# Kernel optimization log

Measured on AMD Instinct MI355X. Metric: run time of the kernel, lower is better.

## Reference

```python
import jax, jax.numpy as jnp
import numpy as np
from jax.scipy.linalg import expm

PROTO_M = 0.99  # hparams['ema_ratio']
NUM_CLASSES = 1000
OUT_DIM = 512
BATCH = 16384


def setup_inputs() -> dict:
    key = jax.random.key(0)
    k1, k2, k3, k4, k5, k6, k7 = jax.random.split(key, 7)
    f = jax.random.normal(k1, (BATCH, OUT_DIM), dtype=jnp.float32)
    f_aug = jax.random.normal(k2, (BATCH, OUT_DIM), dtype=jnp.float32)
    y = jax.random.randint(k3, (BATCH,), 0, NUM_CLASSES, dtype=jnp.int32)
    prototypes = jax.random.normal(k4, (NUM_CLASSES, OUT_DIM), dtype=jnp.float32)
    prototypes_y = jax.random.normal(k5, (NUM_CLASSES, OUT_DIM), dtype=jnp.float32)
    # small positive weights so expm(W*W) stays well-conditioned (DAG weights start near 0)
    weight_pos = jax.random.uniform(k6, (OUT_DIM + 1, OUT_DIM + 1), dtype=jnp.float32) * 0.05
    weight_neg = jax.random.uniform(k7, (OUT_DIM + 1, OUT_DIM + 1), dtype=jnp.float32) * 0.05
    return {"f": f, "f_aug": f_aug, "y": y, "prototypes": prototypes,
            "prototypes_y": prototypes_y, "weight_pos": weight_pos, "weight_neg": weight_neg}


def _l2norm(x, axis=-1, eps=1e-12):
    return x / jnp.maximum(jnp.linalg.norm(x, axis=axis, keepdims=True), eps)


def _ema_scatter(proto, feats, y, num_classes, m):
    # Exact closed form of the sequential per-sample EMA loop:
    # proto_new[c] = proto[c] * m^count(c) + sum_{i: y_i=c} (1-m) * m^{#later same-label} * feats[i]
    B = feats.shape[0]
    onehot = jax.nn.one_hot(y, num_classes, dtype=feats.dtype)          # [B, C]
    counts = onehot.sum(axis=0)                                          # [C]
    cum = jnp.cumsum(onehot, axis=0)                                     # inclusive counts [B, C]
    suffix = counts[y] - cum[jnp.arange(B), y]                           # later same-label count [B]
    w = (1.0 - m) * (m ** suffix)                                        # per-sample EMA weight [B]
    proto_new = proto * (m ** counts)[:, None]
    proto_new = proto_new.at[y].add(w[:, None] * feats)
    return proto_new


def reference(f, f_aug, y, prototypes, prototypes_y, weight_pos, weight_neg):
    D = f.shape[1]
    # dag_mlp mask: expm((W_pos - W_neg)^2)[:dims, -1]
    W = weight_pos - weight_neg
    E = expm(W * W)
    mask = E[:D, -1]                     # [D]
    masked_f_aug = f_aug * mask[None, :]
    nf = _l2norm(f, axis=1)
    nmfa = _l2norm(masked_f_aug, axis=1)
    C = prototypes.shape[0]
    p = _ema_scatter(prototypes, nf, y, C, PROTO_M)
    py = _ema_scatter(prototypes_y, nmfa, y, C, PROTO_M)
    p = _l2norm(p, axis=1)
    py = _l2norm(py, axis=1)
    return (p, py)
```

## Files before the change

kernel.cpp:

```cpp
#include <hip/hip_runtime.h>

#define DP1   513
#define ODIM  512
#define NCLS  1000
#define BATCH 16384
#define MAXC  64
#define MAXW  64
#define L2M   (-0.014499569695115089f)

__global__ __launch_bounds__(256) void mask_kernel(const float* __restrict__ wp,
                                                   const float* __restrict__ wn,
                                                   float* __restrict__ mask) {
    const int wv = threadIdx.x >> 6, lane = threadIdx.x & 63;
    const int i = blockIdx.x * 4 + wv;
    const size_t ro = (size_t)i * DP1;
    float acc = 0.0f;
    for (int j = lane; j < DP1; j += 64) {
        const float w  = wp[ro + j] - wn[ro + j];
        const float wj = wp[(size_t)j * DP1 + (DP1 - 1)] - wn[(size_t)j * DP1 + (DP1 - 1)];
        acc = fmaf(w * w, wj * wj, acc);
    }
#pragma unroll
    for (int off = 32; off > 0; off >>= 1) acc += __shfl_xor(acc, off, 64);
    if (lane == 0) {
        const float w = wp[ro + DP1 - 1] - wn[ro + DP1 - 1];
        mask[i] = fmaf(0.5f, acc, w * w);
    }
}

__global__ __launch_bounds__(256, 4)
void class_kernel(const float* __restrict__ f,
                  const float* __restrict__ f_aug,
                  const int* __restrict__ y,
                  const float* __restrict__ protos,
                  const float* __restrict__ protos_y,
                  const float* __restrict__ mask,
                  float* __restrict__ out) {
    const int c = blockIdx.x;
    const int t = threadIdx.x;
    const int lane = t & 63;
    const int wv = t >> 6;

    __shared__ int   wl[4][MAXW];
    __shared__ int   wcnt[4];
    __shared__ int   s_rows[MAXC];
    __shared__ int   s_off[4], s_cnt;
    __shared__ float sP[4][ODIM], sQ[4][ODIM];
    __shared__ float redA[4], redB[4];

    {
        const unsigned long long mlt = (lane == 0) ? 0ull : ((~0ull) >> (64 - lane));
        int running = 0;
        for (int it = 0; it < 16; ++it) {
            const int base = wv * 4096 + it * 256;
            const int4 yv = ((const int4*)(y + base))[lane];
            const unsigned long long b0 = __ballot(yv.x == c);
            const unsigned long long b1 = __ballot(yv.y == c);
            const unsigned long long b2 = __ballot(yv.z == c);
            const unsigned long long b3 = __ballot(yv.w == c);
            const int cl = __popcll(b0 & mlt) + __popcll(b1 & mlt)
                         + __popcll(b2 & mlt) + __popcll(b3 & mlt);
            int same = 0;
            if (yv.x == c) { int r = running + cl + same; if (r < MAXW) wl[wv][r] = base + 4 * lane + 0; same++; }
            if (yv.y == c) { int r = running + cl + same; if (r < MAXW) wl[wv][r] = base + 4 * lane + 1; same++; }
            if (yv.z == c) { int r = running + cl + same; if (r < MAXW) wl[wv][r] = base + 4 * lane + 2; same++; }
            if (yv.w == c) { int r = running + cl + same; if (r < MAXW) wl[wv][r] = base + 4 * lane + 3; same++; }
            running += __popcll(b0) + __popcll(b1) + __popcll(b2) + __popcll(b3);
        }
        if (lane == 0) wcnt[wv] = (running < MAXW) ? running : MAXW;
    }
    __syncthreads();
    if (t == 0) {
        int o = 0;
#pragma unroll
        for (int w = 0; w < 4; ++w) { s_off[w] = o; o += wcnt[w]; }
        s_cnt = (o < MAXC) ? o : MAXC;
    }
    __syncthreads();
    const int cnt = s_cnt;
    {
        const int o = s_off[wv], n = wcnt[wv];
        for (int k = lane; k < n; k += 64) {
            const int g = o + k;
            if (g < MAXC) s_rows[g] = wl[wv][k];
        }
    }
    __syncthreads();

    const float4 m0 = ((const float4*)mask)[lane];
    const float4 m1 = ((const float4*)mask)[lane + 64];
    float4 aP0 = {0,0,0,0}, aP1 = {0,0,0,0};
    float4 aQ0 = {0,0,0,0}, aQ1 = {0,0,0,0};

    for (int j = wv; j < cnt; j += 4) {
        const int row = s_rows[j];
        const float4* fr = (const float4*)(f + (size_t)row * ODIM);
        const float4* gr = (const float4*)(f_aug + (size_t)row * ODIM);
        const float4 a0 = fr[lane], a1 = fr[lane + 64];
        const float4 g0 = gr[lane], g1 = gr[lane + 64];
        float sA = a0.x*a0.x + a0.y*a0.y + a0.z*a0.z + a0.w*a0.w
                 + a1.x*a1.x + a1.y*a1.y + a1.z*a1.z + a1.w*a1.w;
        const float c0 = g0.x*m0.x, c1 = g0.y*m0.y, c2 = g0.z*m0.z, c3 = g0.w*m0.w;
        const float c4 = g1.x*m1.x, c5 = g1.y*m1.y, c6 = g1.z*m1.z, c7 = g1.w*m1.w;
        float sB = c0*c0 + c1*c1 + c2*c2 + c3*c3 + c4*c4 + c5*c5 + c6*c6 + c7*c7;
#pragma unroll
        for (int off = 32; off > 0; off >>= 1) {
            sA += __shfl_xor(sA, off, 64);
            sB += __shfl_xor(sB, off, 64);
        }
        const float w  = 0.01f * __builtin_exp2f((float)(cnt - 1 - j) * L2M);
        const float wA = w / fmaxf(sqrtf(sA), 1e-12f);
        const float wB = w / fmaxf(sqrtf(sB), 1e-12f);
        aP0.x = fmaf(a0.x, wA, aP0.x); aP0.y = fmaf(a0.y, wA, aP0.y);
        aP0.z = fmaf(a0.z, wA, aP0.z); aP0.w = fmaf(a0.w, wA, aP0.w);
        aP1.x = fmaf(a1.x, wA, aP1.x); aP1.y = fmaf(a1.y, wA, aP1.y);
        aP1.z = fmaf(a1.z, wA, aP1.z); aP1.w = fmaf(a1.w, wA, aP1.w);
        aQ0.x = fmaf(g0.x, wB, aQ0.x); aQ0.y = fmaf(g0.y, wB, aQ0.y);
        aQ0.z = fmaf(g0.z, wB, aQ0.z); aQ0.w = fmaf(g0.w, wB, aQ0.w);
        aQ1.x = fmaf(g1.x, wB, aQ1.x); aQ1.y = fmaf(g1.y, wB, aQ1.y);
        aQ1.z = fmaf(g1.z, wB, aQ1.z); aQ1.w = fmaf(g1.w, wB, aQ1.w);
    }
    ((float4*)sP[wv])[lane]      = aP0;
    ((float4*)sP[wv])[lane + 64] = aP1;
    ((float4*)sQ[wv])[lane]      = aQ0;
    ((float4*)sQ[wv])[lane + 64] = aQ1;
    __syncthreads();

    float P0 = 0.0f, P1 = 0.0f, Q0 = 0.0f, Q1 = 0.0f;
#pragma unroll
    for (int w = 0; w < 4; ++w) {
        P0 += sP[w][t]; P1 += sP[w][t + 256];
        Q0 += sQ[w][t]; Q1 += sQ[w][t + 256];
    }
    const float mc = __builtin_exp2f((float)cnt * L2M);
    const float p0 = fmaf(protos[(size_t)c * ODIM + t],         mc, P0);
    const float p1 = fmaf(protos[(size_t)c * ODIM + t + 256],   mc, P1);
    const float q0 = fmaf(protos_y[(size_t)c * ODIM + t],       mc, mask[t] * Q0);
    const float q1 = fmaf(protos_y[(size_t)c * ODIM + t + 256], mc, mask[t + 256] * Q1);

    float sPn = fmaf(p0, p0, p1 * p1);
    float sQn = fmaf(q0, q0, q1 * q1);
#pragma unroll
    for (int off = 32; off > 0; off >>= 1) {
        sPn += __shfl_xor(sPn, off, 64);
        sQn += __shfl_xor(sQn, off, 64);
    }
    if (lane == 0) { redA[wv] = sPn; redB[wv] = sQn; }
    __syncthreads();
    const float ssP = redA[0] + redA[1] + redA[2] + redA[3];
    const float ssQ = redB[0] + redB[1] + redB[2] + redB[3];
    const float iP = 1.0f / fmaxf(sqrtf(ssP), 1e-12f);
    const float iQ = 1.0f / fmaxf(sqrtf(ssQ), 1e-12f);
    out[(size_t)c * ODIM + t]                       = p0 * iP;
    out[(size_t)c * ODIM + t + 256]                 = p1 * iP;
    out[(size_t)(NCLS + c) * ODIM + t]              = q0 * iQ;
    out[(size_t)(NCLS + c) * ODIM + t + 256]        = q1 * iQ;
}

extern "C" void kernel_launch(void* const* d_in, const int* in_sizes, int n_in,
                              void* d_out, int out_size, void* d_ws, size_t ws_size,
                              hipStream_t stream) {
    const float* f       = (const float*)d_in[0];
    const float* f_aug   = (const float*)d_in[1];
    const int*   y       = (const int*)d_in[2];
    const float* protos  = (const float*)d_in[3];
    const float* protosy = (const float*)d_in[4];
    const float* wp      = (const float*)d_in[5];
    const float* wn      = (const float*)d_in[6];
    float* out = (float*)d_out;

    float* mask = (float*)d_ws;

    mask_kernel<<<128, 256, 0, stream>>>(wp, wn, mask);
    class_kernel<<<NCLS, 256, 0, stream>>>(f, f_aug, y, protos, protosy, mask, out);
}
```

Before: 29.81 us.

## Process each wave's own sample list with prefetch and per-wave EMA scaling

Each wave now accumulates only the samples it found in its own quarter of the batch, so the cross-wave offset computation, the merged row list and two block barriers are removed. EMA weights are built incrementally within a wave by multiplying by 1/m per step and rescaled per wave at the final reduction using the counts of the later waves. The next row's f and f_aug are loaded one iteration ahead to hide global load latency, and the label scan loop is unrolled. The incremental power product can drift slightly from the exact exponent, and the per-wave work is unbalanced when labels cluster in one quarter of the batch.

Result: slower. 32.61 us (+9.4%).

```diff
diff --git a/kernel.cpp b/kernel.cpp
--- a/kernel.cpp
+++ b/kernel.cpp
@@ -4,7 +4,6 @@
 #define ODIM  512
 #define NCLS  1000
 #define BATCH 16384
-#define MAXC  64
 #define MAXW  64
 #define L2M   (-0.014499569695115089f)
 
@@ -43,14 +42,14 @@
 
     __shared__ int   wl[4][MAXW];
     __shared__ int   wcnt[4];
-    __shared__ int   s_rows[MAXC];
-    __shared__ int   s_off[4], s_cnt;
     __shared__ float sP[4][ODIM], sQ[4][ODIM];
     __shared__ float redA[4], redB[4];
 
+    int nw;
     {
         const unsigned long long mlt = (lane == 0) ? 0ull : ((~0ull) >> (64 - lane));
         int running = 0;
+#pragma unroll
         for (int it = 0; it < 16; ++it) {
             const int base = wv * 4096 + it * 256;
             const int4 yv = ((const int4*)(y + base))[lane];
@@ -67,58 +66,53 @@
             if (yv.w == c) { int r = running + cl + same; if (r < MAXW) wl[wv][r] = base + 4 * lane + 3; same++; }
             running += __popcll(b0) + __popcll(b1) + __popcll(b2) + __popcll(b3);
         }
-        if (lane == 0) wcnt[wv] = (running < MAXW) ? running : MAXW;
+        nw = (running < MAXW) ? running : MAXW;
+        if (lane == 0) wcnt[wv] = nw;
     }
-    __syncthreads();
-    if (t == 0) {
-        int o = 0;
-#pragma unroll
-        for (int w = 0; w < 4; ++w) { s_off[w] = o; o += wcnt[w]; }
-        s_cnt = (o < MAXC) ? o : MAXC;
-    }
-    __syncthreads();
-    const int cnt = s_cnt;
-    {
-        const int o = s_off[wv], n = wcnt[wv];
-        for (int k = lane; k < n; k += 64) {
-            const int g = o + k;
-            if (g < MAXC) s_rows[g] = wl[wv][k];
-        }
-    }
-    __syncthreads();
 
     const float4 m0 = ((const float4*)mask)[lane];
     const float4 m1 = ((const float4*)mask)[lane + 64];
     float4 aP0 = {0,0,0,0}, aP1 = {0,0,0,0};
     float4 aQ0 = {0,0,0,0}, aQ1 = {0,0,0,0};
 
-    for (int j = wv; j < cnt; j += 4) {
-        const int row = s_rows[j];
+    if (nw > 0) {
+        int row = wl[wv][0];
         const float4* fr = (const float4*)(f + (size_t)row * ODIM);
         const float4* gr = (const float4*)(f_aug + (size_t)row * ODIM);
-        const float4 a0 = fr[lane], a1 = fr[lane + 64];
-        const float4 g0 = gr[lane], g1 = gr[lane + 64];
-        float sA = a0.x*a0.x + a0.y*a0.y + a0.z*a0.z + a0.w*a0.w
-                 + a1.x*a1.x + a1.y*a1.y + a1.z*a1.z + a1.w*a1.w;
-        const float c0 = g0.x*m0.x, c1 = g0.y*m0.y, c2 = g0.z*m0.z, c3 = g0.w*m0.w;
-        const float c4 = g1.x*m1.x, c5 = g1.y*m1.y, c6 = g1.z*m1.z, c7 = g1.w*m1.w;
-        float sB = c0*c0 + c1*c1 + c2*c2 + c3*c3 + c4*c4 + c5*c5 + c6*c6 + c7*c7;
+        float4 A0 = fr[lane], A1 = fr[lane + 64];
+        float4 G0 = gr[lane], G1 = gr[lane + 64];
+        float pw = 1.0f;
+        const float pinc = 1.0101010101010102f;
+        for (int j = 0; j < nw; ++j) {
+            const int r2 = wl[wv][(j + 1 < nw) ? j + 1 : j];
+            const float4* fr2 = (const float4*)(f + (size_t)r2 * ODIM);
+            const float4* gr2 = (const float4*)(f_aug + (size_t)r2 * ODIM);
+            const float4 B0 = fr2[lane], B1 = fr2[lane + 64];
+            const float4 H0 = gr2[lane], H1 = gr2[lane + 64];
+
+            float sA = A0.x*A0.x + A0.y*A0.y + A0.z*A0.z + A0.w*A0.w
+                     + A1.x*A1.x + A1.y*A1.y + A1.z*A1.z + A1.w*A1.w;
+            const float c0 = G0.x*m0.x, c1 = G0.y*m0.y, c2 = G0.z*m0.z, c3 = G0.w*m0.w;
+            const float c4 = G1.x*m1.x, c5 = G1.y*m1.y, c6 = G1.z*m1.z, c7 = G1.w*m1.w;
+            float sB = c0*c0 + c1*c1 + c2*c2 + c3*c3 + c4*c4 + c5*c5 + c6*c6 + c7*c7;
 #pragma unroll
-        for (int off = 32; off > 0; off >>= 1) {
-            sA += __shfl_xor(sA, off, 64);
-            sB += __shfl_xor(sB, off, 64);
+            for (int off = 32; off > 0; off >>= 1) {
+                sA += __shfl_xor(sA, off, 64);
+                sB += __shfl_xor(sB, off, 64);
+            }
+            const float wA = pw / fmaxf(sqrtf(sA), 1e-12f);
+            const float wB = pw / fmaxf(sqrtf(sB), 1e-12f);
+            aP0.x = fmaf(A0.x, wA, aP0.x); aP0.y = fmaf(A0.y, wA, aP0.y);
+            aP0.z = fmaf(A0.z, wA, aP0.z); aP0.w = fmaf(A0.w, wA, aP0.w);
+            aP1.x = fmaf(A1.x, wA, aP1.x); aP1.y = fmaf(A1.y, wA, aP1.y);
+            aP1.z = fmaf(A1.z, wA, aP1.z); aP1.w = fmaf(A1.w, wA, aP1.w);
+            aQ0.x = fmaf(G0.x, wB, aQ0.x); aQ0.y = fmaf(G0.y, wB, aQ0.y);
+            aQ0.z = fmaf(G0.z, wB, aQ0.z); aQ0.w = fmaf(G0.w, wB, aQ0.w);
+            aQ1.x = fmaf(G1.x, wB, aQ1.x); aQ1.y = fmaf(G1.y, wB, aQ1.y);
+            aQ1.z = fmaf(G1.z, wB, aQ1.z); aQ1.w = fmaf(G1.w, wB, aQ1.w);
+            pw *= pinc;
+            A0 = B0; A1 = B1; G0 = H0; G1 = H1;
         }
-        const float w  = 0.01f * __builtin_exp2f((float)(cnt - 1 - j) * L2M);
-        const float wA = w / fmaxf(sqrtf(sA), 1e-12f);
-        const float wB = w / fmaxf(sqrtf(sB), 1e-12f);
-        aP0.x = fmaf(a0.x, wA, aP0.x); aP0.y = fmaf(a0.y, wA, aP0.y);
-        aP0.z = fmaf(a0.z, wA, aP0.z); aP0.w = fmaf(a0.w, wA, aP0.w);
-        aP1.x = fmaf(a1.x, wA, aP1.x); aP1.y = fmaf(a1.y, wA, aP1.y);
-        aP1.z = fmaf(a1.z, wA, aP1.z); aP1.w = fmaf(a1.w, wA, aP1.w);
-        aQ0.x = fmaf(g0.x, wB, aQ0.x); aQ0.y = fmaf(g0.y, wB, aQ0.y);
-        aQ0.z = fmaf(g0.z, wB, aQ0.z); aQ0.w = fmaf(g0.w, wB, aQ0.w);
-        aQ1.x = fmaf(g1.x, wB, aQ1.x); aQ1.y = fmaf(g1.y, wB, aQ1.y);
-        aQ1.z = fmaf(g1.z, wB, aQ1.z); aQ1.w = fmaf(g1.w, wB, aQ1.w);
     }
     ((float4*)sP[wv])[lane]      = aP0;
     ((float4*)sP[wv])[lane + 64] = aP1;
@@ -126,11 +120,21 @@
     ((float4*)sQ[wv])[lane + 64] = aQ1;
     __syncthreads();
 
+    const int n0 = wcnt[0], n1 = wcnt[1], n2 = wcnt[2], n3 = wcnt[3];
+    const int cnt = n0 + n1 + n2 + n3;
+    float sc[4];
+    sc[0] = 0.01f * __builtin_exp2f((float)(cnt - 1) * L2M);
+    sc[1] = 0.01f * __builtin_exp2f((float)(cnt - 1 - n0) * L2M);
+    sc[2] = 0.01f * __builtin_exp2f((float)(cnt - 1 - n0 - n1) * L2M);
+    sc[3] = 0.01f * __builtin_exp2f((float)(cnt - 1 - n0 - n1 - n2) * L2M);
+
     float P0 = 0.0f, P1 = 0.0f, Q0 = 0.0f, Q1 = 0.0f;
 #pragma unroll
     for (int w = 0; w < 4; ++w) {
-        P0 += sP[w][t]; P1 += sP[w][t + 256];
-        Q0 += sQ[w][t]; Q1 += sQ[w][t + 256];
+        P0 = fmaf(sc[w], sP[w][t],       P0);
+        P1 = fmaf(sc[w], sP[w][t + 256], P1);
+        Q0 = fmaf(sc[w], sQ[w][t],       Q0);
+        Q1 = fmaf(sc[w], sQ[w][t + 256], Q1);
     }
     const float mc = __builtin_exp2f((float)cnt * L2M);
     const float p0 = fmaf(protos[(size_t)c * ODIM + t],         mc, P0);
@@ -151,10 +155,10 @@
     const float ssQ = redB[0] + redB[1] + redB[2] + redB[3];
     const float iP = 1.0f / fmaxf(sqrtf(ssP), 1e-12f);
     const float iQ = 1.0f / fmaxf(sqrtf(ssQ), 1e-12f);
-    out[(size_t)c * ODIM + t]                       = p0 * iP;
-    out[(size_t)c * ODIM + t + 256]                 = p1 * iP;
-    out[(size_t)(NCLS + c) * ODIM + t]              = q0 * iQ;
-    out[(size_t)(NCLS + c) * ODIM + t + 256]        = q1 * iQ;
+    out[(size_t)c * ODIM + t]                = p0 * iP;
+    out[(size_t)c * ODIM + t + 256]          = p1 * iP;
+    out[(size_t)(NCLS + c) * ODIM + t]       = q0 * iQ;
+    out[(size_t)(NCLS + c) * ODIM + t + 256] = q1 * iQ;
 }
 
 extern "C" void kernel_launch(void* const* d_in, const int* in_sizes, int n_in,
```

## Fuse mask and class kernels into one launch with flag-based inter-block sync

Applied to the files above, without the earlier changes.

Merges the DAG-mask computation and the per-class EMA/normalize kernel into one launch. The first 128 blocks compute the mask and publish per-block magic flags with release stores. The class blocks scan labels first, then spin with acquire loads until all flags are set. This is meant to remove the second kernel launch and overlap the label scan with the mask work. It also unrolls the label-scan loop and raises the occupancy hint. The flags are never reset, so on repeated calls the class blocks can read a mask left over from an earlier call instead of waiting. Correctness therefore leans on the workspace persisting across calls and on the mask blocks actually being scheduled.

Measured after the change: 84.27 us. 183% more time.

```diff
diff --git a/kernel.cpp b/kernel.cpp
--- a/kernel.cpp
+++ b/kernel.cpp
@@ -7,40 +7,51 @@
 #define MAXC  64
 #define MAXW  64
 #define L2M   (-0.014499569695115089f)
-
-__global__ __launch_bounds__(256) void mask_kernel(const float* __restrict__ wp,
-                                                   const float* __restrict__ wn,
-                                                   float* __restrict__ mask) {
-    const int wv = threadIdx.x >> 6, lane = threadIdx.x & 63;
-    const int i = blockIdx.x * 4 + wv;
-    const size_t ro = (size_t)i * DP1;
-    float acc = 0.0f;
-    for (int j = lane; j < DP1; j += 64) {
-        const float w  = wp[ro + j] - wn[ro + j];
-        const float wj = wp[(size_t)j * DP1 + (DP1 - 1)] - wn[(size_t)j * DP1 + (DP1 - 1)];
-        acc = fmaf(w * w, wj * wj, acc);
-    }
-#pragma unroll
-    for (int off = 32; off > 0; off >>= 1) acc += __shfl_xor(acc, off, 64);
-    if (lane == 0) {
-        const float w = wp[ro + DP1 - 1] - wn[ro + DP1 - 1];
-        mask[i] = fmaf(0.5f, acc, w * w);
-    }
-}
-
-__global__ __launch_bounds__(256, 4)
-void class_kernel(const float* __restrict__ f,
+#define NMB   128
+#define MAGIC1 0x51F15EEDu
+#define MAGIC2 0x7A3B9C21u
+
+__global__ __launch_bounds__(256, 5)
+void fused_kernel(const float* __restrict__ f,
                   const float* __restrict__ f_aug,
                   const int* __restrict__ y,
                   const float* __restrict__ protos,
                   const float* __restrict__ protos_y,
-                  const float* __restrict__ mask,
+                  const float* __restrict__ wp,
+                  const float* __restrict__ wn,
+                  float* __restrict__ mask,
+                  unsigned int* __restrict__ flags,
                   float* __restrict__ out) {
-    const int c = blockIdx.x;
+    const int b = blockIdx.x;
     const int t = threadIdx.x;
     const int lane = t & 63;
     const int wv = t >> 6;
 
+    if (b < NMB) {
+        const int i = b * 4 + wv;
+        const size_t ro = (size_t)i * DP1;
+        float acc = 0.0f;
+        for (int j = lane; j < DP1; j += 64) {
+            const float w  = wp[ro + j] - wn[ro + j];
+            const float wj = wp[(size_t)j * DP1 + (DP1 - 1)] - wn[(size_t)j * DP1 + (DP1 - 1)];
+            acc = fmaf(w * w, wj * wj, acc);
+        }
+#pragma unroll
+        for (int off = 32; off > 0; off >>= 1) acc += __shfl_xor(acc, off, 64);
+        if (lane == 0) {
+            const float w = wp[ro + DP1 - 1] - wn[ro + DP1 - 1];
+            mask[i] = fmaf(0.5f, acc, w * w);
+        }
+        __syncthreads();
+        if (t == 0) {
+            __threadfence();
+            __hip_atomic_store(&flags[b],       MAGIC1, __ATOMIC_RELEASE, __HIP_MEMORY_SCOPE_AGENT);
+            __hip_atomic_store(&flags[NMB + b], MAGIC2, __ATOMIC_RELEASE, __HIP_MEMORY_SCOPE_AGENT);
+        }
+        return;
+    }
+
+    const int c = b - NMB;
     __shared__ int   wl[4][MAXW];
     __shared__ int   wcnt[4];
     __shared__ int   s_rows[MAXC];
@@ -51,6 +62,7 @@
     {
         const unsigned long long mlt = (lane == 0) ? 0ull : ((~0ull) >> (64 - lane));
         int running = 0;
+#pragma unroll
         for (int it = 0; it < 16; ++it) {
             const int base = wv * 4096 + it * 256;
             const int4 yv = ((const int4*)(y + base))[lane];
@@ -85,6 +97,19 @@
             if (g < MAXC) s_rows[g] = wl[wv][k];
         }
     }
+
+    if (wv == 0) {
+        const int l2 = lane << 1;
+        for (;;) {
+            const unsigned a  = __hip_atomic_load(&flags[l2],           __ATOMIC_ACQUIRE, __HIP_MEMORY_SCOPE_AGENT);
+            const unsigned b2 = __hip_atomic_load(&flags[l2 + 1],       __ATOMIC_ACQUIRE, __HIP_MEMORY_SCOPE_AGENT);
+            const unsigned c2 = __hip_atomic_load(&flags[NMB + l2],     __ATOMIC_ACQUIRE, __HIP_MEMORY_SCOPE_AGENT);
+            const unsigned d  = __hip_atomic_load(&flags[NMB + l2 + 1], __ATOMIC_ACQUIRE, __HIP_MEMORY_SCOPE_AGENT);
+            if (__all(a == MAGIC1 && b2 == MAGIC1 && c2 == MAGIC2 && d == MAGIC2)) break;
+            __builtin_amdgcn_s_sleep(16);
+        }
+        __threadfence();
+    }
     __syncthreads();
 
     const float4 m0 = ((const float4*)mask)[lane];
@@ -151,10 +176,10 @@
     const float ssQ = redB[0] + redB[1] + redB[2] + redB[3];
     const float iP = 1.0f / fmaxf(sqrtf(ssP), 1e-12f);
     const float iQ = 1.0f / fmaxf(sqrtf(ssQ), 1e-12f);
-    out[(size_t)c * ODIM + t]                       = p0 * iP;
-    out[(size_t)c * ODIM + t + 256]                 = p1 * iP;
-    out[(size_t)(NCLS + c) * ODIM + t]              = q0 * iQ;
-    out[(size_t)(NCLS + c) * ODIM + t + 256]        = q1 * iQ;
+    out[(size_t)c * ODIM + t]                = p0 * iP;
+    out[(size_t)c * ODIM + t + 256]          = p1 * iP;
+    out[(size_t)(NCLS + c) * ODIM + t]       = q0 * iQ;
+    out[(size_t)(NCLS + c) * ODIM + t + 256] = q1 * iQ;
 }
 
 extern "C" void kernel_launch(void* const* d_in, const int* in_sizes, int n_in,
@@ -169,8 +194,9 @@
     const float* wn      = (const float*)d_in[6];
     float* out = (float*)d_out;
 
-    float* mask = (float*)d_ws;
-
-    mask_kernel<<<128, 256, 0, stream>>>(wp, wn, mask);
-    class_kernel<<<NCLS, 256, 0, stream>>>(f, f_aug, y, protos, protosy, mask, out);
+    float*        mask  = (float*)d_ws;
+    unsigned int* flags = (unsigned int*)((float*)d_ws + 1024);
+
+    fused_kernel<<<NMB + NCLS, 256, 0, stream>>>(f, f_aug, y, protos, protosy,
+                                                 wp, wn, mask, flags, out);
 }
```
